# Performance work log

Measured on AMD Instinct MI355X. Metric: run time of the kernel, lower is better.

Reference implementation:

```python
import jax, jax.numpy as jnp
import numpy as np

ALPHA_F, GAMMA_F = 0.25, 2.0   # focal loss params
SMOOTH = 1e-6                  # dice smooth
THETA = 5.0                    # boundary weight
W_FOCAL, W_DICE, W_BOUND = 0.3, 0.4, 0.3


def _erode(m):
    # one iteration of scipy binary_erosion, cross (connectivity-1) structure,
    # border_value=0 (outside treated as False)
    p = jnp.pad(m, ((0, 0), (0, 0), (1, 1), (1, 1)), constant_values=False)
    c = p[:, :, 1:-1, 1:-1]
    up = p[:, :, :-2, 1:-1]
    dn = p[:, :, 2:, 1:-1]
    lf = p[:, :, 1:-1, :-2]
    rt = p[:, :, 1:-1, 2:]
    return c & up & dn & lf & rt


def _dilate(m):
    # one iteration of scipy binary_dilation, cross structure, border_value=0
    p = jnp.pad(m, ((0, 0), (0, 0), (1, 1), (1, 1)), constant_values=False)
    c = p[:, :, 1:-1, 1:-1]
    up = p[:, :, :-2, 1:-1]
    dn = p[:, :, 2:, 1:-1]
    lf = p[:, :, 1:-1, :-2]
    rt = p[:, :, 1:-1, 2:]
    return c | up | dn | lf | rt


def setup_inputs() -> dict:
    key = jax.random.key(0)
    k1, k2 = jax.random.split(key)
    B, C, H, W = 64, 1, 512, 512
    inputs = jax.random.normal(k1, (B, C, H, W), dtype=jnp.float32)
    targets = jax.random.randint(k2, (B, C, H, W), 0, 2).astype(jnp.float32)
    return {"inputs": inputs, "targets": targets}


def reference(inputs, targets):
    # numerically stable BCE-with-logits, elementwise
    bce = jnp.maximum(inputs, 0.0) - inputs * targets + jnp.log1p(jnp.exp(-jnp.abs(inputs)))

    # --- focal loss ---
    pt = jnp.exp(-bce)
    focal_loss = jnp.mean(ALPHA_F * (1.0 - pt) ** GAMMA_F * bce)

    # --- dice loss ---
    p = jax.nn.sigmoid(inputs)
    intersection = jnp.sum(p * targets)
    dice = (2.0 * intersection + SMOOTH) / (jnp.sum(p) + jnp.sum(targets) + SMOOTH)
    dice_loss = 1.0 - dice

    # --- boundary-weighted BCE ---
    mask = targets > 0.5
    eroded = _erode(_erode(mask))      # iterations=2
    dilated = _dilate(_dilate(mask))   # iterations=2
    boundary = dilated & (~eroded)
    weights = boundary.astype(jnp.float32) * THETA + 1.0
    boundary_loss = jnp.mean(bce * weights)

    return W_FOCAL * focal_loss + W_DICE * dice_loss + W_BOUND * boundary_loss
```

## Files before the change

### kernel.cpp

```cpp
#include <hip/hip_runtime.h>
#include <math.h>

static constexpr int Hdim = 512;
static constexpr int Wdim = 512;
static constexpr int HW   = Hdim * Wdim;
static constexpr int NIMG = 64;
static constexpr int WPR  = Wdim / 64;
static constexpr int TOTAL_WORDS = NIMG * Hdim * WPR;
static constexpr int RSTRIP = 32;
static constexpr int SPI  = Hdim / RSTRIP;
static constexpr int NBLK = NIMG * SPI;
static constexpr int MROWS = RSTRIP + 4;
static constexpr int NBLK_A = 2048;
static constexpr int NIT = (RSTRIP * Wdim) / (256 * 4);


__global__ __launch_bounds__(256) void mask_kernel(
    const float* __restrict__ tgt, unsigned long long* __restrict__ mask)
{
    const int lane = threadIdx.x & 63;
    const int wid  = (blockIdx.x * 256 + threadIdx.x) >> 6;
    #pragma unroll
    for (int g = 0; g < 8; g++) {
        int w0 = wid * 32 + g * 4;
        float v0 = tgt[(w0 + 0) * 64 + lane];
        float v1 = tgt[(w0 + 1) * 64 + lane];
        float v2 = tgt[(w0 + 2) * 64 + lane];
        float v3 = tgt[(w0 + 3) * 64 + lane];
        unsigned long long m0 = __ballot(v0 > 0.5f);
        unsigned long long m1 = __ballot(v1 > 0.5f);
        unsigned long long m2 = __ballot(v2 > 0.5f);
        unsigned long long m3 = __ballot(v3 > 0.5f);
        if (lane == 0) {
            mask[w0 + 0] = m0;
            mask[w0 + 1] = m1;
            mask[w0 + 2] = m2;
            mask[w0 + 3] = m3;
        }
    }
}

__device__ __forceinline__ unsigned long long shl1(unsigned long long c, unsigned long long l) {
    return (c << 1) | (l >> 63);
}
__device__ __forceinline__ unsigned long long shr1(unsigned long long c, unsigned long long r) {
    return (c >> 1) | (r << 63);
}
__device__ __forceinline__ unsigned long long shl2(unsigned long long c, unsigned long long l) {
    return (c << 2) | (l >> 62);
}
__device__ __forceinline__ unsigned long long shr2(unsigned long long c, unsigned long long r) {
    return (c >> 2) | (r << 62);
}

__global__ __launch_bounds__(256) void combined_loss_kernel(
    const float* __restrict__ inp, const unsigned long long* __restrict__ mask,
    float* __restrict__ partials)
{
    __shared__ unsigned long long tmask[MROWS][WPR];
    __shared__ unsigned long long bmask[RSTRIP][WPR];
    __shared__ float smem[4][5];

    const int img   = blockIdx.x / SPI;
    const int strip = blockIdx.x % SPI;
    const int r0    = strip * RSTRIP;
    const float* ib = inp + img * HW;
    const unsigned long long* mb = mask + img * Hdim * WPR;

    const int wave = threadIdx.x >> 6;
    const int lane = threadIdx.x & 63;

    #pragma unroll
    for (int c = threadIdx.x; c < MROWS * WPR; c += 256) {
        int row  = c >> 3;
        int word = c & 7;
        int gr   = r0 - 2 + row;
        unsigned long long v = 0ULL;
        if ((unsigned)gr < (unsigned)Hdim) v = mb[gr * WPR + word];
        tmask[row][word] = v;
    }
    __syncthreads();

    {
        int row  = threadIdx.x >> 3;
        int word = threadIdx.x & 7;
        int mr = row + 2;

        #define CW(r)  tmask[r][word]
        #define LW(r)  (word > 0 ? tmask[r][word - 1] : 0ULL)
        #define RW(r)  (word < WPR - 1 ? tmask[r][word + 1] : 0ULL)
        unsigned long long c0 = CW(mr),   l0 = LW(mr),   rr0 = RW(mr);
        unsigned long long cm = CW(mr-1), lm = LW(mr-1), rm  = RW(mr-1);
        unsigned long long cp = CW(mr+1), lp = LW(mr+1), rp  = RW(mr+1);
        unsigned long long cm2 = CW(mr-2);
        unsigned long long cp2 = CW(mr+2);
        #undef CW
        #undef LW
        #undef RW

        unsigned long long er =
            c0 & shl1(c0,l0) & shr1(c0,rr0) & shl2(c0,l0) & shr2(c0,rr0)
               & cm & shl1(cm,lm) & shr1(cm,rm)
               & cp & shl1(cp,lp) & shr1(cp,rp)
               & cm2 & cp2;
        unsigned long long di =
            c0 | shl1(c0,l0) | shr1(c0,rr0) | shl2(c0,l0) | shr2(c0,rr0)
               | cm | shl1(cm,lm) | shr1(cm,rm)
               | cp | shl1(cp,lp) | shr1(cp,rp)
               | cm2 | cp2;
        bmask[row][word] = di & ~er;
    }
    __syncthreads();

    float s_focal = 0.f, s_inter = 0.f, s_p = 0.f, s_bw = 0.f;
    int s_tc = 0;

    const float* base = ib + r0 * Wdim + threadIdx.x * 4;
    float4 cur = *(const float4*)(base);
    #pragma unroll
    for (int it = 0; it < NIT; it++) {
        float4 nxt;
        if (it + 1 < NIT) nxt = *(const float4*)(base + (it + 1) * 1024);

        int flat = it * 1024 + threadIdx.x * 4;
        int row  = flat >> 9;
        int x    = flat & (Wdim - 1);
        unsigned int tb4 = (unsigned int)((tmask[row + 2][x >> 6] >> (x & 63)) & 0xFULL);
        unsigned int bb4 = (unsigned int)((bmask[row][x >> 6]     >> (x & 63)) & 0xFULL);
        s_tc += __popc(tb4);
        const float xs[4] = {cur.x, cur.y, cur.z, cur.w};
        #pragma unroll
        for (int k = 0; k < 4; k++) {
            float xi = xs[k];
            bool tpos = (tb4 >> k) & 1;
            float e  = __expf(-fabsf(xi));
            float bce = fmaxf(xi, 0.f) - (tpos ? xi : 0.f) + __logf(1.f + e);
            float rden = __builtin_amdgcn_rcpf(1.f + e);
            float p = (xi >= 0.f ? 1.f : e) * rden;
            float pt = tpos ? p : 1.f - p;
            float om = 1.f - pt;
            s_focal += 0.25f * om * om * bce;
            s_p     += p;
            s_inter += tpos ? p : 0.f;
            float wgt = ((bb4 >> k) & 1) ? 6.0f : 1.0f;
            s_bw += bce * wgt;
        }
        cur = nxt;
    }
    float s_t = (float)s_tc;

    #pragma unroll
    for (int off = 32; off > 0; off >>= 1) {
        s_focal += __shfl_down(s_focal, off);
        s_inter += __shfl_down(s_inter, off);
        s_p     += __shfl_down(s_p,     off);
        s_t     += __shfl_down(s_t,     off);
        s_bw    += __shfl_down(s_bw,    off);
    }
    if (lane == 0) {
        smem[wave][0] = s_focal; smem[wave][1] = s_inter; smem[wave][2] = s_p;
        smem[wave][3] = s_t;     smem[wave][4] = s_bw;
    }
    __syncthreads();
    if (threadIdx.x < 5) {
        float a = smem[0][threadIdx.x] + smem[1][threadIdx.x]
                + smem[2][threadIdx.x] + smem[3][threadIdx.x];
        partials[blockIdx.x * 8 + threadIdx.x] = a;
    }
}

__global__ __launch_bounds__(256) void finalize_kernel(
    const float* __restrict__ partials, float* __restrict__ out)
{
    __shared__ float smem[4][5];
    float a0 = 0.f, a1 = 0.f, a2 = 0.f, a3 = 0.f, a4 = 0.f;
    for (int b = threadIdx.x; b < NBLK; b += 256) {
        const float* s = partials + b * 8;
        a0 += s[0]; a1 += s[1]; a2 += s[2]; a3 += s[3]; a4 += s[4];
    }
    #pragma unroll
    for (int off = 32; off > 0; off >>= 1) {
        a0 += __shfl_down(a0, off);
        a1 += __shfl_down(a1, off);
        a2 += __shfl_down(a2, off);
        a3 += __shfl_down(a3, off);
        a4 += __shfl_down(a4, off);
    }
    int wave = threadIdx.x >> 6;
    int lane = threadIdx.x & 63;
    if (lane == 0) {
        smem[wave][0] = a0; smem[wave][1] = a1; smem[wave][2] = a2;
        smem[wave][3] = a3; smem[wave][4] = a4;
    }
    __syncthreads();
    if (threadIdx.x == 0) {
        double b0 = 0, b1 = 0, b2 = 0, b3 = 0, b4 = 0;
        #pragma unroll
        for (int w = 0; w < 4; w++) {
            b0 += smem[w][0]; b1 += smem[w][1]; b2 += smem[w][2];
            b3 += smem[w][3]; b4 += smem[w][4];
        }
        double invN = 1.0 / (double)(NIMG * HW);
        double focal_loss = b0 * invN;
        double dice = (2.0 * b1 + 1e-6) / (b2 + b3 + 1e-6);
        double boundary_loss = b4 * invN;
        out[0] = (float)(0.3 * focal_loss + 0.4 * (1.0 - dice) + 0.3 * boundary_loss);
    }
}

extern "C" void kernel_launch(void* const* d_in, const int* in_sizes, int n_in,
                              void* d_out, int out_size, void* d_ws, size_t ws_size,
                              hipStream_t stream) {
    const float* inp = (const float*)d_in[0];
    const float* tgt = (const float*)d_in[1];
    float* out = (float*)d_out;
    float* partials = (float*)d_ws;
    unsigned long long* mask = (unsigned long long*)((char*)d_ws + 65536);

    mask_kernel<<<NBLK_A, 256, 0, stream>>>(tgt, mask);
    combined_loss_kernel<<<NBLK, 256, 0, stream>>>(inp, mask, partials);
    finalize_kernel<<<1, 256, 0, stream>>>(partials, out);
}
```

Baseline: 150.4 us.

## Fuse target mask packing into the loss kernel via shared-memory nibbles

Removes the separate mask kernel and its global bitmask round trip. Each loss block now reads its own target rows plus a 2-row halo as float4, thresholds each group of four values into a nibble in shared memory, then packs the nibbles into 64-bit row words. The input prefetch is issued before mask construction so it can overlap. In exchange, halo target rows are read twice (36 rows per 32-row strip), and the kernel does extra shared-memory work and barriers.

```diff
diff --git a/kernel.cpp b/kernel.cpp
--- a/kernel.cpp
+++ b/kernel.cpp
@@ -6,39 +6,15 @@
 static constexpr int HW   = Hdim * Wdim;
 static constexpr int NIMG = 64;
 static constexpr int WPR  = Wdim / 64;
-static constexpr int TOTAL_WORDS = NIMG * Hdim * WPR;
 static constexpr int RSTRIP = 32;
 static constexpr int SPI  = Hdim / RSTRIP;
 static constexpr int NBLK = NIMG * SPI;
 static constexpr int MROWS = RSTRIP + 4;
-static constexpr int NBLK_A = 2048;
+static constexpr int NGRP  = MROWS * (Wdim / 4);
+static constexpr int GPT   = NGRP / 256;
+static constexpr int NWORDS = MROWS * WPR;
 static constexpr int NIT = (RSTRIP * Wdim) / (256 * 4);
 
-
-__global__ __launch_bounds__(256) void mask_kernel(
-    const float* __restrict__ tgt, unsigned long long* __restrict__ mask)
-{
-    const int lane = threadIdx.x & 63;
-    const int wid  = (blockIdx.x * 256 + threadIdx.x) >> 6;
-    #pragma unroll
-    for (int g = 0; g < 8; g++) {
-        int w0 = wid * 32 + g * 4;
-        float v0 = tgt[(w0 + 0) * 64 + lane];
-        float v1 = tgt[(w0 + 1) * 64 + lane];
-        float v2 = tgt[(w0 + 2) * 64 + lane];
-        float v3 = tgt[(w0 + 3) * 64 + lane];
-        unsigned long long m0 = __ballot(v0 > 0.5f);
-        unsigned long long m1 = __ballot(v1 > 0.5f);
-        unsigned long long m2 = __ballot(v2 > 0.5f);
-        unsigned long long m3 = __ballot(v3 > 0.5f);
-        if (lane == 0) {
-            mask[w0 + 0] = m0;
-            mask[w0 + 1] = m1;
-            mask[w0 + 2] = m2;
-            mask[w0 + 3] = m3;
-        }
-    }
-}
 
 __device__ __forceinline__ unsigned long long shl1(unsigned long long c, unsigned long long l) {
     return (c << 1) | (l >> 63);
@@ -53,10 +29,11 @@
     return (c >> 2) | (r << 62);
 }
 
-__global__ __launch_bounds__(256) void combined_loss_kernel(
-    const float* __restrict__ inp, const unsigned long long* __restrict__ mask,
+__global__ __launch_bounds__(256) void fused_loss_kernel(
+    const float* __restrict__ inp, const float* __restrict__ tgt,
     float* __restrict__ partials)
 {
+    __shared__ unsigned int nibw[NGRP / 4];
     __shared__ unsigned long long tmask[MROWS][WPR];
     __shared__ unsigned long long bmask[RSTRIP][WPR];
     __shared__ float smem[4][5];
@@ -65,19 +42,44 @@
     const int strip = blockIdx.x % SPI;
     const int r0    = strip * RSTRIP;
     const float* ib = inp + img * HW;
-    const unsigned long long* mb = mask + img * Hdim * WPR;
+    const float* tb = tgt + img * HW;
 
     const int wave = threadIdx.x >> 6;
     const int lane = threadIdx.x & 63;
 
-    #pragma unroll
-    for (int c = threadIdx.x; c < MROWS * WPR; c += 256) {
-        int row  = c >> 3;
-        int word = c & 7;
-        int gr   = r0 - 2 + row;
-        unsigned long long v = 0ULL;
-        if ((unsigned)gr < (unsigned)Hdim) v = mb[gr * WPR + word];
-        tmask[row][word] = v;
+    const float* base = ib + r0 * Wdim + threadIdx.x * 4;
+    float4 cur = *(const float4*)(base);
+
+    unsigned char* nib = (unsigned char*)nibw;
+    #pragma unroll 6
+    for (int i = 0; i < GPT; i++) {
+        int g   = threadIdx.x + i * 256;
+        int row = g >> 7;
+        int c4  = g & 127;
+        int gr  = r0 - 2 + row;
+        unsigned int n = 0u;
+        if ((unsigned)gr < (unsigned)Hdim) {
+            float4 v = *(const float4*)(tb + gr * Wdim + c4 * 4);
+            n = (unsigned int)(v.x > 0.5f)
+              | ((unsigned int)(v.y > 0.5f) << 1)
+              | ((unsigned int)(v.z > 0.5f) << 2)
+              | ((unsigned int)(v.w > 0.5f) << 3);
+        }
+        nib[g] = (unsigned char)n;
+    }
+    __syncthreads();
+
+    for (int w = threadIdx.x; w < NWORDS; w += 256) {
+        unsigned long long word = 0ULL;
+        #pragma unroll
+        for (int k = 0; k < 4; k++) {
+            unsigned int v = nibw[w * 4 + k];
+            unsigned int y = v | (v >> 4);
+            unsigned int z = y & 0x00FF00FFu;
+            unsigned int h = (z | (z >> 8)) & 0xFFFFu;
+            word |= (unsigned long long)h << (16 * k);
+        }
+        tmask[w >> 3][w & 7] = word;
     }
     __syncthreads();
 
@@ -115,8 +117,6 @@
     float s_focal = 0.f, s_inter = 0.f, s_p = 0.f, s_bw = 0.f;
     int s_tc = 0;
 
-    const float* base = ib + r0 * Wdim + threadIdx.x * 4;
-    float4 cur = *(const float4*)(base);
     #pragma unroll
     for (int it = 0; it < NIT; it++) {
         float4 nxt;
@@ -215,9 +215,7 @@
     const float* tgt = (const float*)d_in[1];
     float* out = (float*)d_out;
     float* partials = (float*)d_ws;
-    unsigned long long* mask = (unsigned long long*)((char*)d_ws + 65536);
-
-    mask_kernel<<<NBLK_A, 256, 0, stream>>>(tgt, mask);
-    combined_loss_kernel<<<NBLK, 256, 0, stream>>>(inp, mask, partials);
+
+    fused_loss_kernel<<<NBLK, 256, 0, stream>>>(inp, tgt, partials);
     finalize_kernel<<<1, 256, 0, stream>>>(partials, out);
 }
```

Result: no change. 150.2 us (-0.1%).
